# Performance work log

Hardware: AMD Instinct MI355X
Metric: run time of the kernel (lower is better)

## Reference

```python
import jax, jax.numpy as jnp
import numpy as np

L, N, E, H, R = 2048, 4, 768, 12, 16
ALPHA = 16.0
LORA_SCALE = ALPHA / R
HEAD_DIM = E // H


def setup_inputs() -> dict:
    rng = jax.random.key(0)
    ks = jax.random.split(rng, 15)
    g = lambda i, shape, s=1.0: jax.random.normal(ks[i], shape, jnp.float32) * s
    return {
        "query": g(0, (L, N, E)),
        "key": g(1, (L, N, E)),
        "value": g(2, (L, N, E)),
        "in_proj_weight": g(3, (3 * E, E), 0.02),
        "in_proj_bias": g(4, (3 * E,), 0.02),
        "q_down": g(5, (R, E), 0.02),
        "q_up": g(6, (E, R), 0.02),
        "k_down": g(7, (R, E), 0.02),
        "k_up": g(8, (E, R), 0.02),
        "v_down": g(9, (R, E), 0.02),
        "v_up": g(10, (E, R), 0.02),
        "out_proj_weight": g(11, (E, E), 0.02),
        "out_proj_bias": g(12, (E,), 0.02),
        "out_down": g(13, (R, E), 0.02),
        "out_up": g(14, (E, R), 0.02),
    }


def _lora_linear(x, W, b, down, up):
    # y = x W^T + b + scale * (x down^T) up^T   (LoRA-adapted nn.Linear)
    return x @ W.T + b + LORA_SCALE * ((x @ down.T) @ up.T)


def reference(query, key, value, in_proj_weight, in_proj_bias,
              q_down, q_up, k_down, k_up, v_down, v_up,
              out_proj_weight, out_proj_bias, out_down, out_up):
    Wq, Wk, Wv = jnp.split(in_proj_weight, 3, axis=0)
    bq, bk, bv = jnp.split(in_proj_bias, 3)
    q = _lora_linear(query, Wq, bq, q_down, q_up)   # (L,N,E)
    k = _lora_linear(key, Wk, bk, k_down, k_up)     # (S,N,E)
    v = _lora_linear(value, Wv, bv, v_down, v_up)

    def to_heads(t):  # (T,N,E) -> (N,H,T,hd)
        return t.reshape(t.shape[0], N, H, HEAD_DIM).transpose(1, 2, 0, 3)

    qh, kh, vh = to_heads(q), to_heads(k), to_heads(v)
    scale = 1.0 / jnp.sqrt(jnp.float32(HEAD_DIM))
    scores = jnp.einsum('nhld,nhsd->nhls', qh * scale, kh)  # (N,H,L,S)
    attn = jax.nn.softmax(scores, axis=-1)
    o = jnp.einsum('nhls,nhsd->nhld', attn, vh)             # (N,H,L,hd)
    o = o.transpose(2, 0, 1, 3).reshape(L, N, E)            # (L,N,E)
    return _lora_linear(o, out_proj_weight, out_proj_bias, out_down, out_up)
```

## Files before the change

kernel.cpp:

```cpp
#include <hip/hip_runtime.h>

#define LL 2048
#define NN 4
#define EE 768
#define HH 12
#define RR 16
#define HD 64
#define TT (LL*NN)
#define F3 (3*EE)
#define KA 832

typedef __bf16 bf16;
typedef bf16 bf16x4 __attribute__((ext_vector_type(4)));
typedef bf16 bf16x8 __attribute__((ext_vector_type(8)));
typedef float floatx4 __attribute__((ext_vector_type(4)));
typedef float floatx16 __attribute__((ext_vector_type(16)));
typedef unsigned uintx4 __attribute__((ext_vector_type(4)));

__global__ __launch_bounds__(256) void cast_x(
    const float* __restrict__ q, const float* __restrict__ k,
    const float* __restrict__ v, bf16* __restrict__ Xa)
{
    const int bid = blockIdx.x;
    const int third = bid / (TT/8);
    const int r0 = (bid % (TT/8)) * 8;
    const float* x = (third == 0) ? q : (third == 1) ? k : v;
    const int tid = threadIdx.x;
    #pragma unroll
    for (int i = 0; i < 6; ++i) {
        const int e4 = i*256 + tid;
        const int row = e4 / 192;
        const int col = (e4 % 192) * 4;
        const float4 f = *(const float4*)(x + (size_t)(r0+row)*EE + col);
        bf16x4 h = { (bf16)f.x, (bf16)f.y, (bf16)f.z, (bf16)f.w };
        *(bf16x4*)(Xa + ((size_t)third*TT + r0 + row)*KA + col) = h;
    }
}

__global__ __launch_bounds__(256) void prep_w(
    const float* __restrict__ W,  const float* __restrict__ qu,
    const float* __restrict__ ku, const float* __restrict__ vu,
    const float* __restrict__ Wo, const float* __restrict__ ou,
    const float* __restrict__ qd, const float* __restrict__ kd,
    const float* __restrict__ vd, const float* __restrict__ odw,
    bf16* __restrict__ Wa, bf16* __restrict__ Dm)
{
    const int f = blockIdx.x;
    const int tid = threadIdx.x;
    if (f < 3072) {
        const float* src;
        const float* up;
        if (f < F3) {
            const int third = f / EE, fe = f % EE;
            src = W + (size_t)f*EE;
            up  = ((third == 0) ? qu : (third == 1) ? ku : vu) + fe*RR;
        } else {
            const int fe = f - F3;
            src = Wo + (size_t)fe*EE;
            up  = ou + fe*RR;
        }
        bf16* row = Wa + (size_t)f*KA;
        #pragma unroll
        for (int i = 0; i < 3; ++i)
            row[i*256 + tid] = (bf16)src[i*256 + tid];
        if (tid < 64)
            row[EE + tid] = (tid < RR) ? (bf16)up[tid] : (bf16)0.f;
    } else {
        const int f2 = f - 3072;
        const int which = f2 >> 4, r = f2 & 15;
        const float* dsrc = (which == 0) ? qd : (which == 1) ? kd
                          : (which == 2) ? vd : odw;
        bf16* drow = Dm + (size_t)f2*EE;
        #pragma unroll
        for (int i = 0; i < 3; ++i)
            drow[i*256 + tid] = (bf16)dsrc[(size_t)r*EE + i*256 + tid];
    }
}

template<int XA>
__global__ __launch_bounds__(256) void lora_rank16(
    bf16* __restrict__ A, const bf16* __restrict__ Dm)
{
    __shared__ float red[4][64][16];
    const int row0 = blockIdx.x * 64;
    const int dn = XA ? (row0 >> 13) : 3;
    const bf16* D = Dm + (size_t)dn*16*EE;
    const int tid = threadIdx.x;
    const int wave = tid >> 6, lane = tid & 63;
    const int quad = lane >> 4, l16 = lane & 15;

    floatx4 acc[4];
    #pragma unroll
    for (int rt = 0; rt < 4; ++rt) acc[rt] = (floatx4){0.f,0.f,0.f,0.f};

    #pragma unroll
    for (int ks = 0; ks < 6; ++ks) {
        const int k0 = wave*192 + ks*32;
        const bf16x8 b = *(const bf16x8*)(D + (size_t)l16*EE + k0 + quad*8);
        #pragma unroll
        for (int rt = 0; rt < 4; ++rt) {
            const bf16x8 a = *(const bf16x8*)(
                A + (size_t)(row0 + rt*16 + l16)*KA + k0 + quad*8);
            acc[rt] = __builtin_amdgcn_mfma_f32_16x16x32_bf16(a, b, acc[rt], 0, 0, 0);
        }
    }

    #pragma unroll
    for (int rt = 0; rt < 4; ++rt)
        #pragma unroll
        for (int rr = 0; rr < 4; ++rr)
            red[wave][rt*16 + quad*4 + rr][l16] = acc[rt][rr];
    __syncthreads();

    {
        const int row = tid >> 2, cq = (tid & 3) * 4;
        bf16x4 o;
        #pragma unroll
        for (int j = 0; j < 4; ++j) {
            const float s = red[0][row][cq+j] + red[1][row][cq+j]
                          + red[2][row][cq+j] + red[3][row][cq+j];
            o[j] = (bf16)s;
        }
        *(bf16x4*)(A + (size_t)(row0+row)*KA + EE + cq) = o;
    }
    #pragma unroll
    for (int p = 0; p < 3; ++p) {
        const int id = p*256 + tid;
        const int row = id / 12, c = id % 12;
        *(bf16x4*)(A + (size_t)(row0+row)*KA + 784 + c*4) = (bf16x4){};
    }
}

template<int MODE>
__global__ __launch_bounds__(256) void gemm_aug(
    const bf16* __restrict__ A,
    const bf16* __restrict__ B,
    const float* __restrict__ bias,
    bf16* __restrict__ qo, bf16* __restrict__ ko, bf16* __restrict__ vo,
    float* __restrict__ fo)
{
    __shared__ bf16 As[128][72];
    __shared__ bf16 Bs[128][72];
    const int t0 = blockIdx.x * 128;
    const int f0 = blockIdx.y * 128;
    const int tid = threadIdx.x;
    const int wave = tid >> 6, lane = tid & 63;
    const int quad = lane >> 4, l16 = lane & 15;
    const int m0 = (wave & 1) * 64;
    const int n0 = (wave >> 1) * 64;

    const int third = (MODE == 0) ? (f0 / EE) : 0;
    const bf16* Aeff = (MODE == 0) ? (A + (size_t)third*TT*KA) : A;

    floatx4 acc[4][4];
    #pragma unroll
    for (int rt = 0; rt < 4; ++rt)
        #pragma unroll
        for (int ct = 0; ct < 4; ++ct) acc[rt][ct] = (floatx4){0.f,0.f,0.f,0.f};

    for (int kb = 0; kb < KA/64; ++kb) {
        __syncthreads();
        #pragma unroll
        for (int c = 0; c < 4; ++c) {
            int id = c*256 + tid;
            int row = id >> 3, cg = id & 7;
            *(bf16x8*)(&As[row][cg*8]) =
                *(const bf16x8*)(Aeff + (size_t)(t0+row)*KA + kb*64 + cg*8);
            *(bf16x8*)(&Bs[row][cg*8]) =
                *(const bf16x8*)(B + (size_t)(f0+row)*KA + kb*64 + cg*8);
        }
        __syncthreads();
        #pragma unroll
        for (int kc = 0; kc < 2; ++kc) {
            bf16x8 a[4], bfr[4];
            #pragma unroll
            for (int rt = 0; rt < 4; ++rt)
                a[rt] = *(const bf16x8*)(&As[m0 + rt*16 + l16][kc*32 + quad*8]);
            #pragma unroll
            for (int ct = 0; ct < 4; ++ct)
                bfr[ct] = *(const bf16x8*)(&Bs[n0 + ct*16 + l16][kc*32 + quad*8]);
            #pragma unroll
            for (int rt = 0; rt < 4; ++rt)
                #pragma unroll
                for (int ct = 0; ct < 4; ++ct)
                    acc[rt][ct] = __builtin_amdgcn_mfma_f32_16x16x32_bf16(
                        a[rt], bfr[ct], acc[rt][ct], 0, 0, 0);
        }
    }

    #pragma unroll
    for (int rt = 0; rt < 4; ++rt) {
        #pragma unroll
        for (int r = 0; r < 4; ++r) {
            const int t = t0 + m0 + rt*16 + quad*4 + r;
            #pragma unroll
            for (int ct = 0; ct < 4; ++ct) {
                const int fl = n0 + ct*16 + l16;
                float c = acc[rt][ct][r] + bias[f0 + fl];
                if (MODE == 0) {
                    const int fe = (f0 % EE) + fl;
                    const int h = fe >> 6, d = fe & 63;
                    const int l = t >> 2, n = t & 3;
                    const size_t idx = (((size_t)(n*HH + h)*LL) + l)*HD + d;
                    if (third == 0)      qo[idx] = (bf16)(c * 0.180336877f);
                    else if (third == 1) ko[idx] = (bf16)c;
                    else                 vo[idx] = (bf16)c;
                } else {
                    fo[(size_t)t*EE + f0 + fl] = c;
                }
            }
        }
    }
}

__global__ __launch_bounds__(256) void vtrans(
    const bf16* __restrict__ vin, bf16* __restrict__ vout)
{
    __shared__ bf16 T[64][64];
    const int nh = blockIdx.x >> 5;
    const int l0 = (blockIdx.x & 31) * 64;
    const int tid = threadIdx.x;
    const bf16* src = vin + ((size_t)nh*LL + l0)*HD;
    #pragma unroll
    for (int c = 0; c < 2; ++c) {
        int id = c*256 + tid;
        int row = id >> 3, dg = id & 7;
        int pg = dg ^ (row & 7);
        *(bf16x8*)(&T[row][pg*8]) = *(const bf16x8*)(src + row*HD + dg*8);
    }
    __syncthreads();
    bf16* dst = vout + (size_t)nh*HD*LL;
    const int wave = tid >> 6, lane = tid & 63;
    #pragma unroll
    for (int it = 0; it < 2; ++it) {
        const int d  = it*32 + wave*8 + (lane >> 3);
        const int cg = lane & 7;
        bf16x8 vv;
        #pragma unroll
        for (int j = 0; j < 8; ++j) {
            const int lrow = cg*8 + j;
            const int pg = (d >> 3) ^ (lrow & 7);
            vv[j] = T[lrow][pg*8 + (d & 7)];
        }
        *(bf16x8*)(dst + (size_t)d*LL + l0 + cg*8) = vv;
    }
}

__device__ __forceinline__ unsigned pk_bf16(float a, float b) {
    unsigned r;
    asm("v_cvt_pk_bf16_f32 %0, %1, %2" : "=v"(r) : "v"(a), "v"(b));
    return r;
}

__global__ __launch_bounds__(256) void attn_mfma(
    const bf16* __restrict__ qf, const bf16* __restrict__ kf,
    const bf16* __restrict__ vf, bf16* __restrict__ Oa)
{
    __shared__ bf16 Ks[2][64][64];
    __shared__ bf16 Vt[2][64][64];
    __shared__ float linv[4][32];

    const int bid = blockIdx.x;
    const int nh = bid % 48;
    const int l0 = (bid / 48) * 128;
    const int tid  = threadIdx.x;
    const int wave = tid >> 6;
    const int lane = tid & 63;
    const int l32  = lane & 31;
    const int hi   = lane >> 5;
    const int sw   = l32 & 7;

    const bf16* qb = qf + (size_t)nh * LL * HD;
    const bf16* kb = kf + (size_t)nh * LL * HD;
    const bf16* vb = vf + (size_t)nh * HD * LL;

    const int q0 = l0 + wave * 32;

    const int rowA = tid >> 3;
    const int rowB = rowA + 32;
    const int g0   = tid & 7;
    const int gsA  = g0 ^ (rowA & 7);

    bf16x8 bq[4];
    #pragma unroll
    for (int t = 0; t < 4; ++t)
        bq[t] = *(const bf16x8*)(qb + (size_t)(q0 + l32)*HD + t*16 + hi*8);

    floatx16 oacc0 = {0,0,0,0, 0,0,0,0, 0,0,0,0, 0,0,0,0};
    floatx16 oacc1 = {0,0,0,0, 0,0,0,0, 0,0,0,0, 0,0,0,0};
    float lsum = 0.f;

    bf16x8 gk0, gk1, gv0, gv1;

#define LOADT(S) do {                                                         \
        gk0 = *(const bf16x8*)(kb + (size_t)((S)+rowA)*HD + g0*8);            \
        gk1 = *(const bf16x8*)(kb + (size_t)((S)+rowB)*HD + g0*8);            \
        gv0 = *(const bf16x8*)(vb + (size_t)rowA*LL + (S) + g0*8);            \
        gv1 = *(const bf16x8*)(vb + (size_t)rowB*LL + (S) + g0*8);            \
    } while (0)
#define STORET(B) do {                                                        \
        *(bf16x8*)(&Ks[B][rowA][gsA*8]) = gk0;                                \
        *(bf16x8*)(&Ks[B][rowB][gsA*8]) = gk1;                                \
        *(bf16x8*)(&Vt[B][rowA][gsA*8]) = gv0;                                \
        *(bf16x8*)(&Vt[B][rowB][gsA*8]) = gv1;                                \
    } while (0)

    LOADT(0);
    STORET(0);
    LOADT(64);
    __syncthreads();

    for (int t = 0; t < 32; ++t) {
        const int b = t & 1;
        if (t + 1 < 32) STORET(b ^ 1);
        if (t + 2 < 32) LOADT((t + 2) * 64);

        #pragma unroll
        for (int ss = 0; ss < 2; ++ss) {
            bf16x8 ak[4];
            #pragma unroll
            for (int t4 = 0; t4 < 4; ++t4)
                ak[t4] = *(const bf16x8*)(
                    &Ks[b][ss*32 + l32][((t4*2 + hi) ^ sw) * 8]);

            floatx16 sacc = {0,0,0,0, 0,0,0,0, 0,0,0,0, 0,0,0,0};
            #pragma unroll
            for (int t4 = 0; t4 < 4; ++t4)
                sacc = __builtin_amdgcn_mfma_f32_32x32x16_bf16(
                    ak[t4], bq[t4], sacc, 0, 0, 0);

            bf16x8 bv[4];
            #pragma unroll
            for (int tl = 0; tl < 2; ++tl)
                #pragma unroll
                for (int dt = 0; dt < 2; ++dt)
                    bv[tl*2 + dt] = *(const bf16x8*)(
                        &Vt[b][dt*32 + l32][((ss*4 + tl*2 + hi) ^ sw) * 8]);

            float p[16];
            #pragma unroll
            for (int r = 0; r < 16; ++r) {
                p[r] = __builtin_exp2f(sacc[r]);
                lsum += p[r];
            }

            union { uintx4 u; bf16x8 h; } fr0, fr1;
            {
                unsigned c0 = pk_bf16(p[0], p[1]);
                unsigned c1 = pk_bf16(p[2], p[3]);
                unsigned c2 = pk_bf16(p[4], p[5]);
                unsigned c3 = pk_bf16(p[6], p[7]);
                asm("v_permlane32_swap_b32 %0, %1" : "+v"(c0), "+v"(c2));
                asm("v_permlane32_swap_b32 %0, %1" : "+v"(c1), "+v"(c3));
                fr0.u = (uintx4){c0, c1, c2, c3};
            }
            {
                unsigned c0 = pk_bf16(p[8],  p[9]);
                unsigned c1 = pk_bf16(p[10], p[11]);
                unsigned c2 = pk_bf16(p[12], p[13]);
                unsigned c3 = pk_bf16(p[14], p[15]);
                asm("v_permlane32_swap_b32 %0, %1" : "+v"(c0), "+v"(c2));
                asm("v_permlane32_swap_b32 %0, %1" : "+v"(c1), "+v"(c3));
                fr1.u = (uintx4){c0, c1, c2, c3};
            }

            oacc0 = __builtin_amdgcn_mfma_f32_32x32x16_bf16(fr0.h, bv[0], oacc0, 0, 0, 0);
            oacc1 = __builtin_amdgcn_mfma_f32_32x32x16_bf16(fr0.h, bv[1], oacc1, 0, 0, 0);
            oacc0 = __builtin_amdgcn_mfma_f32_32x32x16_bf16(fr1.h, bv[2], oacc0, 0, 0, 0);
            oacc1 = __builtin_amdgcn_mfma_f32_32x32x16_bf16(fr1.h, bv[3], oacc1, 0, 0, 0);
        }
        __syncthreads();
    }
#undef LOADT
#undef STORET

    lsum += __shfl_xor(lsum, 32, 64);
    if (lane < 32) linv[wave][l32] = 1.f / lsum;

    const int n = nh / HH, h = nh % HH;
    #pragma unroll
    for (int r = 0; r < 16; ++r) {
        const int qloc = (r & 3) + 8*(r >> 2) + 4*hi;
        const float iv = linv[wave][qloc];
        const size_t t = (size_t)(q0 + qloc)*NN + n;
        Oa[t*KA + h*64 + l32]      = (bf16)(oacc0[r] * iv);
        Oa[t*KA + h*64 + 32 + l32] = (bf16)(oacc1[r] * iv);
    }
}

extern "C" void kernel_launch(void* const* d_in, const int* in_sizes, int n_in,
                              void* d_out, int out_size, void* d_ws, size_t ws_size,
                              hipStream_t stream) {
    const float* q   = (const float*)d_in[0];
    const float* k   = (const float*)d_in[1];
    const float* v   = (const float*)d_in[2];
    const float* W   = (const float*)d_in[3];
    const float* b   = (const float*)d_in[4];
    const float* qd  = (const float*)d_in[5];
    const float* qu  = (const float*)d_in[6];
    const float* kd  = (const float*)d_in[7];
    const float* ku  = (const float*)d_in[8];
    const float* vd  = (const float*)d_in[9];
    const float* vu  = (const float*)d_in[10];
    const float* Wo  = (const float*)d_in[11];
    const float* bo  = (const float*)d_in[12];
    const float* odw = (const float*)d_in[13];
    const float* ou  = (const float*)d_in[14];
    float* out = (float*)d_out;

    char* wsb = (char*)d_ws;
    bf16* Xa  = (bf16*)wsb;
    bf16* vfb = (bf16*)wsb;
    bf16* Oa  = (bf16*)(wsb + (size_t)TT*EE*2);
    bf16* Wa  = (bf16*)(wsb + (size_t)3*TT*KA*2);
    bf16* qfb = (bf16*)((char*)Wa + (size_t)3072*KA*2);
    bf16* kfb = qfb + (size_t)TT*EE;
    bf16* vld = kfb + (size_t)TT*EE;
    bf16* Dm  = vld + (size_t)TT*EE;

    cast_x<<<3072, 256, 0, stream>>>(q, k, v, Xa);
    prep_w<<<3136, 256, 0, stream>>>(W, qu, ku, vu, Wo, ou, qd, kd, vd, odw, Wa, Dm);
    lora_rank16<1><<<3*TT/64, 256, 0, stream>>>(Xa, Dm);
    gemm_aug<0><<<dim3(TT/128, F3/128), 256, 0, stream>>>(
        Xa, Wa, b, qfb, kfb, vld, nullptr);
    vtrans<<<48*32, 256, 0, stream>>>(vld, vfb);
    attn_mfma<<<48*16, 256, 0, stream>>>(qfb, kfb, vfb, Oa);
    lora_rank16<0><<<TT/64, 256, 0, stream>>>(Oa, Dm);
    gemm_aug<1><<<dim3(TT/128, EE/128), 256, 0, stream>>>(
        Oa, Wa + (size_t)F3*KA, bo, nullptr, nullptr, nullptr, out);
}
```

Baseline: 318.0 us.

## Compute softmax row sums via MFMA with ones and unroll double-buffer loop

The row-sum of exponentials is now accumulated by two extra MFMA ops against a ones matrix, replacing 16 scalar adds per sub-tile plus the shuffle and shared-memory reduction at the end. The main loop is unrolled by two with separately named A/B LDS buffers and branch-free wraparound prefetch, and launch bounds request 3 blocks per CU. This trades extra matrix-core work and 16 accumulator registers for fewer VALU ops and less control overhead. The sums are taken over bf16-rounded probabilities, which matches what the PV product uses.

```diff
diff --git a/kernel.cpp b/kernel.cpp
--- a/kernel.cpp
+++ b/kernel.cpp
@@ -16,6 +16,8 @@
 typedef float floatx4 __attribute__((ext_vector_type(4)));
 typedef float floatx16 __attribute__((ext_vector_type(16)));
 typedef unsigned uintx4 __attribute__((ext_vector_type(4)));
+
+#define ZERO16 (floatx16){0.f,0.f,0.f,0.f,0.f,0.f,0.f,0.f,0.f,0.f,0.f,0.f,0.f,0.f,0.f,0.f}
 
 __global__ __launch_bounds__(256) void cast_x(
     const float* __restrict__ q, const float* __restrict__ k,
@@ -252,13 +254,73 @@
     return r;
 }
 
-__global__ __launch_bounds__(256) void attn_mfma(
+__device__ __forceinline__ void compute_tile(
+    const bf16 (&KS)[64][64], const bf16 (&VS)[64][64],
+    const bf16x8 (&bq)[4], const bf16x8& ones, const floatx16& z16,
+    int l32, int hi, int sw,
+    floatx16& oacc0, floatx16& oacc1, floatx16& oaccS)
+{
+    #pragma unroll
+    for (int ss = 0; ss < 2; ++ss) {
+        bf16x8 ak[4];
+        #pragma unroll
+        for (int t4 = 0; t4 < 4; ++t4)
+            ak[t4] = *(const bf16x8*)(&KS[ss*32 + l32][((t4*2 + hi) ^ sw) * 8]);
+
+        floatx16 sacc = __builtin_amdgcn_mfma_f32_32x32x16_bf16(
+            ak[0], bq[0], z16, 0, 0, 0);
+        #pragma unroll
+        for (int t4 = 1; t4 < 4; ++t4)
+            sacc = __builtin_amdgcn_mfma_f32_32x32x16_bf16(
+                ak[t4], bq[t4], sacc, 0, 0, 0);
+
+        bf16x8 bv[4];
+        #pragma unroll
+        for (int tl = 0; tl < 2; ++tl)
+            #pragma unroll
+            for (int dt = 0; dt < 2; ++dt)
+                bv[tl*2 + dt] = *(const bf16x8*)(
+                    &VS[dt*32 + l32][((ss*4 + tl*2 + hi) ^ sw) * 8]);
+
+        float p[16];
+        #pragma unroll
+        for (int r = 0; r < 16; ++r) p[r] = __builtin_exp2f(sacc[r]);
+
+        union { uintx4 u; bf16x8 h; } fr0, fr1;
+        {
+            unsigned c0 = pk_bf16(p[0], p[1]);
+            unsigned c1 = pk_bf16(p[2], p[3]);
+            unsigned c2 = pk_bf16(p[4], p[5]);
+            unsigned c3 = pk_bf16(p[6], p[7]);
+            asm("v_permlane32_swap_b32 %0, %1" : "+v"(c0), "+v"(c2));
+            asm("v_permlane32_swap_b32 %0, %1" : "+v"(c1), "+v"(c3));
+            fr0.u = (uintx4){c0, c1, c2, c3};
+        }
+        {
+            unsigned c0 = pk_bf16(p[8],  p[9]);
+            unsigned c1 = pk_bf16(p[10], p[11]);
+            unsigned c2 = pk_bf16(p[12], p[13]);
+            unsigned c3 = pk_bf16(p[14], p[15]);
+            asm("v_permlane32_swap_b32 %0, %1" : "+v"(c0), "+v"(c2));
+            asm("v_permlane32_swap_b32 %0, %1" : "+v"(c1), "+v"(c3));
+            fr1.u = (uintx4){c0, c1, c2, c3};
+        }
+
+        oaccS = __builtin_amdgcn_mfma_f32_32x32x16_bf16(fr0.h, ones, oaccS, 0, 0, 0);
+        oaccS = __builtin_amdgcn_mfma_f32_32x32x16_bf16(fr1.h, ones, oaccS, 0, 0, 0);
+        oacc0 = __builtin_amdgcn_mfma_f32_32x32x16_bf16(fr0.h, bv[0], oacc0, 0, 0, 0);
+        oacc1 = __builtin_amdgcn_mfma_f32_32x32x16_bf16(fr0.h, bv[1], oacc1, 0, 0, 0);
+        oacc0 = __builtin_amdgcn_mfma_f32_32x32x16_bf16(fr1.h, bv[2], oacc0, 0, 0, 0);
+        oacc1 = __builtin_amdgcn_mfma_f32_32x32x16_bf16(fr1.h, bv[3], oacc1, 0, 0, 0);
+    }
+}
+
+__global__ __launch_bounds__(256, 3) void attn_mfma(
     const bf16* __restrict__ qf, const bf16* __restrict__ kf,
     const bf16* __restrict__ vf, bf16* __restrict__ Oa)
 {
-    __shared__ bf16 Ks[2][64][64];
-    __shared__ bf16 Vt[2][64][64];
-    __shared__ float linv[4][32];
+    __shared__ bf16 KsA[64][64], VtA[64][64];
+    __shared__ bf16 KsB[64][64], VtB[64][64];
 
     const int bid = blockIdx.x;
     const int nh = bid % 48;
@@ -281,107 +343,69 @@
     const int g0   = tid & 7;
     const int gsA  = g0 ^ (rowA & 7);
 
+    const bf16* pK0 = kb + (size_t)rowA*HD + g0*8;
+    const bf16* pK1 = kb + (size_t)rowB*HD + g0*8;
+    const bf16* pV0 = vb + (size_t)rowA*LL + g0*8;
+    const bf16* pV1 = vb + (size_t)rowB*LL + g0*8;
+
     bf16x8 bq[4];
     #pragma unroll
     for (int t = 0; t < 4; ++t)
         bq[t] = *(const bf16x8*)(qb + (size_t)(q0 + l32)*HD + t*16 + hi*8);
 
-    floatx16 oacc0 = {0,0,0,0, 0,0,0,0, 0,0,0,0, 0,0,0,0};
-    floatx16 oacc1 = {0,0,0,0, 0,0,0,0, 0,0,0,0, 0,0,0,0};
-    float lsum = 0.f;
+    const bf16x8 ones = { (bf16)1.f, (bf16)1.f, (bf16)1.f, (bf16)1.f,
+                          (bf16)1.f, (bf16)1.f, (bf16)1.f, (bf16)1.f };
+    const floatx16 z16 = ZERO16;
+
+    floatx16 oacc0 = ZERO16;
+    floatx16 oacc1 = ZERO16;
+    floatx16 oaccS = ZERO16;
 
     bf16x8 gk0, gk1, gv0, gv1;
 
 #define LOADT(S) do {                                                         \
-        gk0 = *(const bf16x8*)(kb + (size_t)((S)+rowA)*HD + g0*8);            \
-        gk1 = *(const bf16x8*)(kb + (size_t)((S)+rowB)*HD + g0*8);            \
-        gv0 = *(const bf16x8*)(vb + (size_t)rowA*LL + (S) + g0*8);            \
-        gv1 = *(const bf16x8*)(vb + (size_t)rowB*LL + (S) + g0*8);            \
+        gk0 = *(const bf16x8*)(pK0 + (size_t)(S)*HD);                         \
+        gk1 = *(const bf16x8*)(pK1 + (size_t)(S)*HD);                         \
+        gv0 = *(const bf16x8*)(pV0 + (S));                                    \
+        gv1 = *(const bf16x8*)(pV1 + (S));                                    \
     } while (0)
-#define STORET(B) do {                                                        \
-        *(bf16x8*)(&Ks[B][rowA][gsA*8]) = gk0;                                \
-        *(bf16x8*)(&Ks[B][rowB][gsA*8]) = gk1;                                \
-        *(bf16x8*)(&Vt[B][rowA][gsA*8]) = gv0;                                \
-        *(bf16x8*)(&Vt[B][rowB][gsA*8]) = gv1;                                \
+#define STORE_A() do {                                                        \
+        *(bf16x8*)(&KsA[rowA][gsA*8]) = gk0;                                  \
+        *(bf16x8*)(&KsA[rowB][gsA*8]) = gk1;                                  \
+        *(bf16x8*)(&VtA[rowA][gsA*8]) = gv0;                                  \
+        *(bf16x8*)(&VtA[rowB][gsA*8]) = gv1;                                  \
     } while (0)
+#define STORE_B() do {                                                        \
+        *(bf16x8*)(&KsB[rowA][gsA*8]) = gk0;                                  \
+        *(bf16x8*)(&KsB[rowB][gsA*8]) = gk1;                                  \
+        *(bf16x8*)(&VtB[rowA][gsA*8]) = gv0;                                  \
+        *(bf16x8*)(&VtB[rowB][gsA*8]) = gv1;                                  \
+    } while (0)
 
     LOADT(0);
-    STORET(0);
+    STORE_A();
     LOADT(64);
     __syncthreads();
 
-    for (int t = 0; t < 32; ++t) {
-        const int b = t & 1;
-        if (t + 1 < 32) STORET(b ^ 1);
-        if (t + 2 < 32) LOADT((t + 2) * 64);
-
-        #pragma unroll
-        for (int ss = 0; ss < 2; ++ss) {
-            bf16x8 ak[4];
-            #pragma unroll
-            for (int t4 = 0; t4 < 4; ++t4)
-                ak[t4] = *(const bf16x8*)(
-                    &Ks[b][ss*32 + l32][((t4*2 + hi) ^ sw) * 8]);
-
-            floatx16 sacc = {0,0,0,0, 0,0,0,0, 0,0,0,0, 0,0,0,0};
-            #pragma unroll
-            for (int t4 = 0; t4 < 4; ++t4)
-                sacc = __builtin_amdgcn_mfma_f32_32x32x16_bf16(
-                    ak[t4], bq[t4], sacc, 0, 0, 0);
-
-            bf16x8 bv[4];
-            #pragma unroll
-            for (int tl = 0; tl < 2; ++tl)
-                #pragma unroll
-                for (int dt = 0; dt < 2; ++dt)
-                    bv[tl*2 + dt] = *(const bf16x8*)(
-                        &Vt[b][dt*32 + l32][((ss*4 + tl*2 + hi) ^ sw) * 8]);
-
-            float p[16];
-            #pragma unroll
-            for (int r = 0; r < 16; ++r) {
-                p[r] = __builtin_exp2f(sacc[r]);
-                lsum += p[r];
-            }
-
-            union { uintx4 u; bf16x8 h; } fr0, fr1;
-            {
-                unsigned c0 = pk_bf16(p[0], p[1]);
-                unsigned c1 = pk_bf16(p[2], p[3]);
-                unsigned c2 = pk_bf16(p[4], p[5]);
-                unsigned c3 = pk_bf16(p[6], p[7]);
-                asm("v_permlane32_swap_b32 %0, %1" : "+v"(c0), "+v"(c2));
-                asm("v_permlane32_swap_b32 %0, %1" : "+v"(c1), "+v"(c3));
-                fr0.u = (uintx4){c0, c1, c2, c3};
-            }
-            {
-                unsigned c0 = pk_bf16(p[8],  p[9]);
-                unsigned c1 = pk_bf16(p[10], p[11]);
-                unsigned c2 = pk_bf16(p[12], p[13]);
-                unsigned c3 = pk_bf16(p[14], p[15]);
-                asm("v_permlane32_swap_b32 %0, %1" : "+v"(c0), "+v"(c2));
-                asm("v_permlane32_swap_b32 %0, %1" : "+v"(c1), "+v"(c3));
-                fr1.u = (uintx4){c0, c1, c2, c3};
-            }
-
-            oacc0 = __builtin_amdgcn_mfma_f32_32x32x16_bf16(fr0.h, bv[0], oacc0, 0, 0, 0);
-            oacc1 = __builtin_amdgcn_mfma_f32_32x32x16_bf16(fr0.h, bv[1], oacc1, 0, 0, 0);
-            oacc0 = __builtin_amdgcn_mfma_f32_32x32x16_bf16(fr1.h, bv[2], oacc0, 0, 0, 0);
-            oacc1 = __builtin_amdgcn_mfma_f32_32x32x16_bf16(fr1.h, bv[3], oacc1, 0, 0, 0);
-        }
+    for (int tt = 0; tt < 16; ++tt) {
+        STORE_B();
+        LOADT((size_t)((2*tt + 2) & 31) * 64);
+        compute_tile(KsA, VtA, bq, ones, z16, l32, hi, sw, oacc0, oacc1, oaccS);
         __syncthreads();
+        STORE_A();
+        LOADT((size_t)((2*tt + 3) & 31) * 64);
+        compute_tile(KsB, VtB, bq, ones, z16, l32, hi, sw, oacc0, oacc1, oaccS);
+        __syncthreads();
     }
 #undef LOADT
-#undef STORET
-
-    lsum += __shfl_xor(lsum, 32, 64);
-    if (lane < 32) linv[wave][l32] = 1.f / lsum;
+#undef STORE_A
+#undef STORE_B
 
     const int n = nh / HH, h = nh % HH;
     #pragma unroll
     for (int r = 0; r < 16; ++r) {
         const int qloc = (r & 3) + 8*(r >> 2) + 4*hi;
-        const float iv = linv[wave][qloc];
+        const float iv = 1.f / oaccS[r];
         const size_t t = (size_t)(q0 + qloc)*NN + n;
         Oa[t*KA + h*64 + l32]      = (bf16)(oacc0[r] * iv);
         Oa[t*KA + h*64 + 32 + l32] = (bf16)(oacc1[r] * iv);
```

Result: no change. 312.6 us (-1.7%).
